# Optimization experiments

Hardware: AMD Instinct MI355X
Metric: run time of the kernel (lower is better)

Reference implementation:

```python
import jax, jax.numpy as jnp
import numpy as np

K = 20
NEG = 0.2      # leaky relu slope
EPS = 1e-5     # layernorm eps


def knn(x, k=K):
    # x: [B, C, N] -> neighbor indices [B, N, k] by largest negative sq-distance
    xt = jnp.swapaxes(x, 1, 2)                      # [B, N, C]
    inner = -2.0 * jnp.einsum('bnc,bcm->bnm', xt, x)
    xx = jnp.sum(x * x, axis=1)                     # [B, N]
    pd = -xx[:, :, None] - inner - xx[:, None, :]   # [B, N, N]
    _, idx = jax.lax.top_k(pd, k)
    return idx


def graph_feature(x, k=K):
    # x: [B, C, N] -> edge features [B, 2C, N, k] = cat(neighbor - center, center)
    xt = jnp.swapaxes(x, 1, 2)                      # [B, N, C]
    idx = knn(x, k)                                 # [B, N, k]
    nbr = jax.vmap(lambda f, i: f[i])(xt, idx)      # [B, N, k, C]
    ctr = jnp.broadcast_to(xt[:, :, None, :], nbr.shape)
    feat = jnp.concatenate([nbr - ctr, ctr], axis=-1)
    return jnp.transpose(feat, (0, 3, 1, 2))


def lrelu(x):
    return jnp.where(x >= 0, x, NEG * x)


def conv1x1(x, w):
    # x: [B, C, N, k], w: [O, C]  (BatchNorm2d in eval with default stats == identity)
    return jnp.einsum('oc,bcnk->bonk', w, x)


def layernorm(x, g, b):
    m = jnp.mean(x, axis=-1, keepdims=True)
    v = jnp.var(x, axis=-1, keepdims=True)
    return (x - m) * jax.lax.rsqrt(v + EPS) * g + b


def l2n(x):
    return x / jnp.linalg.norm(x, axis=1, keepdims=True)


def fc_layer(x, w, bias, g, beta):
    # l2-normalize -> Linear -> LayerNorm -> LeakyReLU (fc_layer with norm=True, bn=True)
    x = l2n(x)
    x = x @ w.T
    if bias is not None:
        x = x + bias
    return lrelu(layernorm(x, g, beta))


def transform_net(f0, tw1, tw2, tw3, tfc1_w, tfc1_g, tfc1_b, tfc2_w, tfc2_bias, tfc2_g, tfc2_b, tfc3_w, tfc3_b):
    # f0: [B, 6, N, k]
    h = lrelu(conv1x1(f0, tw1))                     # [B, 64, N, k]
    h = lrelu(conv1x1(h, tw2))                      # [B, 128, N, k]
    h = jnp.max(h, axis=-1, keepdims=True)          # [B, 128, N, 1]
    h = lrelu(conv1x1(h, tw3))                      # [B, 1024, N, 1]
    h = jnp.max(h, axis=2)[:, :, 0]                 # [B, 1024]
    h = fc_layer(h, tfc1_w, None, tfc1_g, tfc1_b)   # dgcnn: fc1 bias=False
    h = fc_layer(h, tfc2_w, tfc2_bias, tfc2_g, tfc2_b)
    h = h @ tfc3_w.T + tfc3_b                       # [B, 9]
    h = h + jnp.eye(3, dtype=h.dtype).reshape(9)
    return h.reshape(-1, 3, 3)


def setup_inputs() -> dict:
    key = jax.random.key(0)
    ks = jax.random.split(key, 16)

    def w(k, o, i):
        return jax.random.normal(k, (o, i), dtype=jnp.float32) / np.sqrt(i)

    inp = {
        'x': jax.random.normal(ks[0], (16, 3, 1024), dtype=jnp.float32),
        # transform_net params
        'tw1': w(ks[1], 64, 6),
        'tw2': w(ks[2], 128, 64),
        'tw3': w(ks[3], 1024, 128),
        'tfc1_w': w(ks[4], 512, 1024),
        'tfc1_g': jnp.ones((512,), jnp.float32),
        'tfc1_b': jnp.zeros((512,), jnp.float32),
        'tfc2_w': w(ks[5], 256, 512),
        'tfc2_bias': jnp.zeros((256,), jnp.float32),
        'tfc2_g': jnp.ones((256,), jnp.float32),
        'tfc2_b': jnp.zeros((256,), jnp.float32),
        'tfc3_w': w(ks[6], 9, 256) * 0.01,
        'tfc3_b': jnp.zeros((9,), jnp.float32),
        # EdgeConv params (1x1 convs, bias=False for dgcnn)
        'w1': w(ks[7], 64, 6),
        'w2': w(ks[8], 64, 128),
        'w3': w(ks[9], 128, 128),
        'w4': w(ks[10], 256, 256),
        'w5': w(ks[11], 1024, 512),
    }
    return inp


def reference(x, tw1, tw2, tw3, tfc1_w, tfc1_g, tfc1_b, tfc2_w, tfc2_bias, tfc2_g, tfc2_b,
              tfc3_w, tfc3_b, w1, w2, w3, w4, w5):
    # spatial transform from first graph feature
    f0 = graph_feature(x)                           # [B, 6, N, k]
    t = transform_net(f0, tw1, tw2, tw3, tfc1_w, tfc1_g, tfc1_b,
                      tfc2_w, tfc2_bias, tfc2_g, tfc2_b, tfc3_w, tfc3_b)
    x = jnp.einsum('bij,bjn->bin', t, x)            # [B, 3, N]

    # 4 EdgeConv blocks: graph_feature -> 1x1 conv (+BN identity) -> lrelu -> max over k
    x1 = jnp.max(lrelu(conv1x1(graph_feature(x), w1)), axis=-1)    # [B, 64, N]
    x2 = jnp.max(lrelu(conv1x1(graph_feature(x1), w2)), axis=-1)   # [B, 64, N]
    x3 = jnp.max(lrelu(conv1x1(graph_feature(x2), w3)), axis=-1)   # [B, 128, N]
    x4 = jnp.max(lrelu(conv1x1(graph_feature(x3), w4)), axis=-1)   # [B, 256, N]

    xc = jnp.concatenate([x1, x2, x3, x4], axis=1)  # [B, 512, N]
    x5 = lrelu(jnp.einsum('oc,bcn->bon', w5, xc))   # [B, 1024, N]
    return jnp.max(x5, axis=-1)                     # [B, 1024] global feature
```

## Files before the change

kernel.cpp:

```cpp
#include <hip/hip_runtime.h>
#include <math.h>

#define BATCH 16
#define NPTS 1024
#define KNN 20

__device__ __forceinline__ float lrelu(float v) { return v >= 0.f ? v : 0.2f * v; }

typedef __attribute__((ext_vector_type(8))) short bf16x8;
typedef __attribute__((ext_vector_type(4))) float f32x4;

__device__ __forceinline__ ushort f2bf(float f) {
  union { float f; unsigned u; } v; v.f = f;
  unsigned r = (v.u + 0x7FFFu + ((v.u >> 16) & 1u)) >> 16;
  return (ushort)r;
}

__device__ __forceinline__ unsigned wave_min_u32(unsigned v) {
  unsigned t;
  t = (unsigned)__builtin_amdgcn_update_dpp((int)v, (int)v, 0x111, 0xf, 0xf, false);
  v = t < v ? t : v;
  t = (unsigned)__builtin_amdgcn_update_dpp((int)v, (int)v, 0x112, 0xf, 0xf, false);
  v = t < v ? t : v;
  t = (unsigned)__builtin_amdgcn_update_dpp((int)v, (int)v, 0x114, 0xf, 0xf, false);
  v = t < v ? t : v;
  t = (unsigned)__builtin_amdgcn_update_dpp((int)v, (int)v, 0x118, 0xf, 0xf, false);
  v = t < v ? t : v;
  t = (unsigned)__builtin_amdgcn_update_dpp((int)v, (int)v, 0x142, 0xf, 0xf, false);
  v = t < v ? t : v;
  t = (unsigned)__builtin_amdgcn_update_dpp((int)v, (int)v, 0x143, 0xf, 0xf, false);
  v = t < v ? t : v;
  return (unsigned)__builtin_amdgcn_readlane((int)v, 63);
}

__global__ __launch_bounds__(256)
void prep_all_kernel(const float* __restrict__ tw1, const float* __restrict__ w1,
                     const float* __restrict__ w2, const float* __restrict__ w3,
                     const float* __restrict__ w4, const float* __restrict__ w5,
                     const float* __restrict__ tw2, const float* __restrict__ tw3,
                     float* __restrict__ tw1aT, float* __restrict__ tw1dT,
                     float* __restrict__ w1aT, float* __restrict__ w1dT,
                     float* __restrict__ w2aT, float* __restrict__ w2dT,
                     float* __restrict__ w3aT, float* __restrict__ w3dT,
                     ushort* __restrict__ w4a_bf, ushort* __restrict__ w4d_bf,
                     ushort* __restrict__ w5_bf,
                     float* __restrict__ tw2T, float* __restrict__ tw3T) {
  int g = blockIdx.x * 256 + threadIdx.x;
  if (g < 524288) { w5_bf[g] = f2bf(w5[g]); return; }
  g -= 524288;
  if (g < 131072) { int c = g >> 10, o = g & 1023; tw3T[g] = tw3[o * 128 + c]; return; }
  g -= 131072;
  if (g < 32768) {
    int o = g >> 7, c = g & 127;
    float a = w4[o * 256 + c], bb = w4[o * 256 + 128 + c];
    w4a_bf[g] = f2bf(a); w4d_bf[g] = f2bf(bb - a);
    return;
  }
  g -= 32768;
  if (g < 8192) {
    int c = g >> 7, o = g & 127;
    float a = w3[o * 128 + c], bb = w3[o * 128 + 64 + c];
    w3aT[g] = a; w3dT[g] = bb - a;
    return;
  }
  g -= 8192;
  if (g < 8192) { int c = g >> 7, o = g & 127; tw2T[g] = tw2[o * 64 + c]; return; }
  g -= 8192;
  if (g < 4096) {
    int c = g >> 6, o = g & 63;
    float a = w2[o * 128 + c], bb = w2[o * 128 + 64 + c];
    w2aT[g] = a; w2dT[g] = bb - a;
    return;
  }
  g -= 4096;
  if (g < 192) {
    int c = g >> 6, o = g & 63;
    float a = tw1[o * 6 + c], bb = tw1[o * 6 + 3 + c];
    tw1aT[g] = a; tw1dT[g] = bb - a;
    return;
  }
  g -= 192;
  if (g < 192) {
    int c = g >> 6, o = g & 63;
    float a = w1[o * 6 + c], bb = w1[o * 6 + 3 + c];
    w1aT[g] = a; w1dT[g] = bb - a;
  }
}

template<int C, int NO>
__global__ __launch_bounds__(256)
void knn_dual_kernel(const float* __restrict__ X, long sxb,
                     const float* __restrict__ xx, int* __restrict__ idxout,
                     const float* __restrict__ WaT, const float* __restrict__ WdT,
                     int ldW, float* __restrict__ outY, float* __restrict__ outZ,
                     long sob, int son) {
  __shared__ __align__(16) char smem[16384];
  const int gid = blockIdx.x;
  const int tid = threadIdx.x;

  if (gid < 1024) {
    float (*sc4)[NPTS] = reinterpret_cast<float (*)[NPTS]>(smem);
    const int b = gid >> 6, i0 = (gid & 63) * 16;
    const float* Xb = X + (size_t)b * sxb;
    const int j0 = tid * 4;
    float acc[16][4];
    #pragma unroll
    for (int q = 0; q < 16; ++q)
      #pragma unroll
      for (int u = 0; u < 4; ++u) acc[q][u] = 0.f;
    float4 xxjv = make_float4(0.f, 0.f, 0.f, 0.f);
    for (int c = 0; c < C; ++c) {
      const float4 xv = *reinterpret_cast<const float4*>(Xb + (size_t)c * NPTS + j0);
      if (C == 3) {
        xxjv.x = fmaf(xv.x, xv.x, xxjv.x);
        xxjv.y = fmaf(xv.y, xv.y, xxjv.y);
        xxjv.z = fmaf(xv.z, xv.z, xxjv.z);
        xxjv.w = fmaf(xv.w, xv.w, xxjv.w);
      }
      const float* xr = Xb + (size_t)c * NPTS + i0;
      #pragma unroll
      for (int q = 0; q < 16; ++q) {
        const float xiq = xr[q];
        acc[q][0] = fmaf(xiq, xv.x, acc[q][0]);
        acc[q][1] = fmaf(xiq, xv.y, acc[q][1]);
        acc[q][2] = fmaf(xiq, xv.z, acc[q][2]);
        acc[q][3] = fmaf(xiq, xv.w, acc[q][3]);
      }
    }
    float4 xxj;
    if (C == 3) xxj = xxjv;
    else xxj = *reinterpret_cast<const float4*>(xx + b * NPTS + j0);
    const int wv = tid >> 6, lane = tid & 63;
    unsigned ku[4][16];

    #pragma unroll
    for (int r = 0; r < 4; ++r) {
      if (r > 0) __syncthreads();
      #pragma unroll
      for (int q = 0; q < 4; ++q) {
        const int qq = r * 4 + q;
        float4 st;
        st.x = fmaf(-2.f, acc[qq][0], xxj.x);
        st.y = fmaf(-2.f, acc[qq][1], xxj.y);
        st.z = fmaf(-2.f, acc[qq][2], xxj.z);
        st.w = fmaf(-2.f, acc[qq][3], xxj.w);
        *reinterpret_cast<float4*>(&sc4[q][j0]) = st;
      }
      __syncthreads();
      #pragma unroll
      for (int s = 0; s < 16; ++s) {
        const unsigned u = __float_as_uint(sc4[wv][lane + 64 * s]);
        ku[r][s] = u ^ ((unsigned)((int)u >> 31) | 0x80000000u);
      }
    }

    unsigned c1s[4], c2s[4]; int c1j[4], c2j[4];
    #pragma unroll
    for (int r = 0; r < 4; ++r) {
      unsigned b1 = 0xFFFFFFFFu, b2 = 0xFFFFFFFFu; int s1 = 0, s2 = 0;
      #pragma unroll
      for (int s = 0; s < 16; ++s) {
        const unsigned k = ku[r][s];
        const bool a1 = k < b1, a2 = k < b2;
        const unsigned n1 = a1 ? k : b1;  const int ns1 = a1 ? s : s1;
        const unsigned n2 = a1 ? b1 : (a2 ? k : b2);
        const int ns2 = a1 ? s1 : (a2 ? s : s2);
        b1 = n1; s1 = ns1; b2 = n2; s2 = ns2;
      }
      c1s[r] = b1; c1j[r] = lane + (s1 << 6);
      c2s[r] = b2; c2j[r] = lane + (s2 << 6);
    }
    const unsigned INVS = 0xFFFFFFFFu;
    int my[4] = {0, 0, 0, 0};
    for (int t = 0; t < KNN; ++t) {
      unsigned ws[4]; int wl[4], jw[4];
      #pragma unroll
      for (int r = 0; r < 4; ++r) ws[r] = wave_min_u32(c1s[r]);
      #pragma unroll
      for (int r = 0; r < 4; ++r) wl[r] = __ffsll((long long)__ballot(c1s[r] == ws[r])) - 1;
      #pragma unroll
      for (int r = 0; r < 4; ++r) jw[r] = __builtin_amdgcn_readlane(c1j[r], wl[r]);
      if (lane == t) {
        #pragma unroll
        for (int r = 0; r < 4; ++r) my[r] = jw[r];
      }
      bool cons = false;
      #pragma unroll
      for (int r = 0; r < 4; ++r) {
        const bool win = (lane == wl[r]);
        c1s[r] = win ? c2s[r] : c1s[r];
        c1j[r] = win ? c2j[r] : c1j[r];
        c2s[r] = win ? INVS : c2s[r];
        cons = cons || (c1s[r] == INVS);
      }
      if (__any(cons)) {
        #pragma unroll
        for (int r = 0; r < 4; ++r) {
          if (c1s[r] == INVS) {
            unsigned m1 = INVS, m2 = INVS; int r1 = 0, r2 = 0;
            #pragma unroll
            for (int s = 0; s < 16; ++s) {
              const unsigned k = ku[r][s];
              const bool ok = k > ws[r];
              const bool a1 = ok && (k < m1), a2 = ok && (k < m2);
              const unsigned nm1 = a1 ? k : m1;  const int nr1 = a1 ? s : r1;
              const unsigned nm2 = a1 ? m1 : (a2 ? k : m2);
              const int nr2 = a1 ? r1 : (a2 ? s : r2);
              m1 = nm1; r1 = nr1; m2 = nm2; r2 = nr2;
            }
            c1s[r] = (m1 == INVS) ? 0xFFFFFFFEu : m1;  c1j[r] = lane + (r1 << 6);
            c2s[r] = (m2 == INVS) ? 0xFFFFFFFEu : m2;  c2j[r] = lane + (r2 << 6);
          }
        }
      }
    }
    if (lane < KNN) {
      #pragma unroll
      for (int r = 0; r < 4; ++r)
        idxout[(size_t)(b * NPTS + i0 + r * 4 + wv) * KNN + lane] = my[r];
    }
  } else {
    float (*Xs)[64]  = reinterpret_cast<float (*)[64]>(smem);
    float (*Was)[64] = reinterpret_cast<float (*)[64]>(smem + 4096);
    float (*Wds)[64] = reinterpret_cast<float (*)[64]>(smem + 8192);
    const int g2 = gid - 1024;
    const int bx = g2 & 15;
    const int rest = g2 >> 4;
    const int oy = rest % NO;
    const int b = rest / NO;
    const int n0 = bx * 64, o0 = oy * 64;
    const int lr = tid & 63;
    const int c4 = (tid >> 6) * 4;
    const int tn = tid & 15, to = tid >> 4;
    float accY[4][4], accZ[4][4];
    #pragma unroll
    for (int i = 0; i < 4; ++i)
      #pragma unroll
      for (int j = 0; j < 4; ++j) { accY[i][j] = 0.f; accZ[i][j] = 0.f; }

    const size_t xbase = (size_t)b * sxb;
    for (int k0 = 0; k0 < C; k0 += 16) {
      #pragma unroll
      for (int u = 0; u < 4; ++u) {
        int c = k0 + c4 + u;
        float xv = 0.f, wa = 0.f, wd = 0.f;
        if (c < C) {
          xv = X[xbase + (size_t)(n0 + lr) + (size_t)c * NPTS];
          wa = WaT[(size_t)c * ldW + o0 + lr];
          wd = WdT[(size_t)c * ldW + o0 + lr];
        }
        Xs[c4 + u][lr] = xv;
        Was[c4 + u][lr] = wa;
        Wds[c4 + u][lr] = wd;
      }
      __syncthreads();
      #pragma unroll
      for (int kk = 0; kk < 16; ++kk) {
        const float4 xa = *reinterpret_cast<const float4*>(&Xs[kk][tn * 4]);
        const float4 wav = *reinterpret_cast<const float4*>(&Was[kk][to * 4]);
        const float4 wdv = *reinterpret_cast<const float4*>(&Wds[kk][to * 4]);
        const float xr[4] = {xa.x, xa.y, xa.z, xa.w};
        const float war[4] = {wav.x, wav.y, wav.z, wav.w};
        const float wdr[4] = {wdv.x, wdv.y, wdv.z, wdv.w};
        #pragma unroll
        for (int i = 0; i < 4; ++i)
          #pragma unroll
          for (int j = 0; j < 4; ++j) {
            accY[i][j] = fmaf(xr[i], war[j], accY[i][j]);
            accZ[i][j] = fmaf(xr[i], wdr[j], accZ[i][j]);
          }
      }
      __syncthreads();
    }
    #pragma unroll
    for (int i = 0; i < 4; ++i) {
      const size_t base = (size_t)b * sob + (size_t)(n0 + tn * 4 + i) * son + o0 + to * 4;
      *reinterpret_cast<float4*>(&outY[base]) =
        make_float4(accY[i][0], accY[i][1], accY[i][2], accY[i][3]);
      *reinterpret_cast<float4*>(&outZ[base]) =
        make_float4(accZ[i][0], accZ[i][1], accZ[i][2], accZ[i][3]);
    }
  }
}

__global__ __launch_bounds__(256)
void knn_mfma_kernel(const float* __restrict__ Xt, long sxb,
                     const float* __restrict__ xx, int* __restrict__ idxout,
                     const ushort* __restrict__ Xg,
                     const ushort* __restrict__ w4a, const ushort* __restrict__ w4d,
                     float* __restrict__ ybuf, float* __restrict__ zbuf) {
  __shared__ __align__(16) char smem[32768];
  const int gid = blockIdx.x;
  const int tid = threadIdx.x;

  if (gid < 1024) {
    float (*sc4)[NPTS] = reinterpret_cast<float (*)[NPTS]>(smem);
    const int b = gid >> 6, i0 = (gid & 63) * 16;
    const float* Xb = Xt + (size_t)b * sxb;
    const int j0 = tid * 4;
    float acc[16][4];
    #pragma unroll
    for (int q = 0; q < 16; ++q)
      #pragma unroll
      for (int u = 0; u < 4; ++u) acc[q][u] = 0.f;
    for (int c = 0; c < 128; ++c) {
      const float4 xv = *reinterpret_cast<const float4*>(Xb + (size_t)c * NPTS + j0);
      const float* xr = Xb + (size_t)c * NPTS + i0;
      #pragma unroll
      for (int q = 0; q < 16; ++q) {
        const float xiq = xr[q];
        acc[q][0] = fmaf(xiq, xv.x, acc[q][0]);
        acc[q][1] = fmaf(xiq, xv.y, acc[q][1]);
        acc[q][2] = fmaf(xiq, xv.z, acc[q][2]);
        acc[q][3] = fmaf(xiq, xv.w, acc[q][3]);
      }
    }
    const float4 xxj = *reinterpret_cast<const float4*>(xx + b * NPTS + j0);
    const int wv = tid >> 6, lane = tid & 63;
    unsigned ku[4][16];
    #pragma unroll
    for (int r = 0; r < 4; ++r) {
      if (r > 0) __syncthreads();
      #pragma unroll
      for (int q = 0; q < 4; ++q) {
        const int qq = r * 4 + q;
        float4 st;
        st.x = fmaf(-2.f, acc[qq][0], xxj.x);
        st.y = fmaf(-2.f, acc[qq][1], xxj.y);
        st.z = fmaf(-2.f, acc[qq][2], xxj.z);
        st.w = fmaf(-2.f, acc[qq][3], xxj.w);
        *reinterpret_cast<float4*>(&sc4[q][j0]) = st;
      }
      __syncthreads();
      #pragma unroll
      for (int s = 0; s < 16; ++s) {
        const unsigned u = __float_as_uint(sc4[wv][lane + 64 * s]);
        ku[r][s] = u ^ ((unsigned)((int)u >> 31) | 0x80000000u);
      }
    }
    unsigned c1s[4], c2s[4]; int c1j[4], c2j[4];
    #pragma unroll
    for (int r = 0; r < 4; ++r) {
      unsigned b1 = 0xFFFFFFFFu, b2 = 0xFFFFFFFFu; int s1 = 0, s2 = 0;
      #pragma unroll
      for (int s = 0; s < 16; ++s) {
        const unsigned k = ku[r][s];
        const bool a1 = k < b1, a2 = k < b2;
        const unsigned n1 = a1 ? k : b1;  const int ns1 = a1 ? s : s1;
        const unsigned n2 = a1 ? b1 : (a2 ? k : b2);
        const int ns2 = a1 ? s1 : (a2 ? s : s2);
        b1 = n1; s1 = ns1; b2 = n2; s2 = ns2;
      }
      c1s[r] = b1; c1j[r] = lane + (s1 << 6);
      c2s[r] = b2; c2j[r] = lane + (s2 << 6);
    }
    const unsigned INVS = 0xFFFFFFFFu;
    int my[4] = {0, 0, 0, 0};
    for (int t = 0; t < KNN; ++t) {
      unsigned ws[4]; int wl[4], jw[4];
      #pragma unroll
      for (int r = 0; r < 4; ++r) ws[r] = wave_min_u32(c1s[r]);
      #pragma unroll
      for (int r = 0; r < 4; ++r) wl[r] = __ffsll((long long)__ballot(c1s[r] == ws[r])) - 1;
      #pragma unroll
      for (int r = 0; r < 4; ++r) jw[r] = __builtin_amdgcn_readlane(c1j[r], wl[r]);
      if (lane == t) {
        #pragma unroll
        for (int r = 0; r < 4; ++r) my[r] = jw[r];
      }
      bool cons = false;
      #pragma unroll
      for (int r = 0; r < 4; ++r) {
        const bool win = (lane == wl[r]);
        c1s[r] = win ? c2s[r] : c1s[r];
        c1j[r] = win ? c2j[r] : c1j[r];
        c2s[r] = win ? INVS : c2s[r];
        cons = cons || (c1s[r] == INVS);
      }
      if (__any(cons)) {
        #pragma unroll
        for (int r = 0; r < 4; ++r) {
          if (c1s[r] == INVS) {
            unsigned m1 = INVS, m2 = INVS; int r1 = 0, r2 = 0;
            #pragma unroll
            for (int s = 0; s < 16; ++s) {
              const unsigned k = ku[r][s];
              const bool ok = k > ws[r];
              const bool a1 = ok && (k < m1), a2 = ok && (k < m2);
              const unsigned nm1 = a1 ? k : m1;  const int nr1 = a1 ? s : r1;
              const unsigned nm2 = a1 ? m1 : (a2 ? k : m2);
              const int nr2 = a1 ? r1 : (a2 ? s : r2);
              m1 = nm1; r1 = nr1; m2 = nm2; r2 = nr2;
            }
            c1s[r] = (m1 == INVS) ? 0xFFFFFFFEu : m1;  c1j[r] = lane + (r1 << 6);
            c2s[r] = (m2 == INVS) ? 0xFFFFFFFEu : m2;  c2j[r] = lane + (r2 << 6);
          }
        }
      }
    }
    if (lane < KNN) {
      #pragma unroll
      for (int r = 0; r < 4; ++r)
        idxout[(size_t)(b * NPTS + i0 + r * 4 + wv) * KNN + lane] = my[r];
    }
  } else {
    char* As = smem;
    char* Bs = smem + 16384;
    int g2 = gid - 1024;
    const ushort* Wg = (g2 < 256) ? w4a : w4d;
    float* outp = (g2 < 256) ? ybuf : zbuf;
    g2 &= 255;
    const int bx = g2 & 7, oy = (g2 >> 3) & 1, b = g2 >> 4;
    const int n0 = bx * 128, o0 = oy * 128;
    const int lane = tid & 63;
    const int wrow = (tid >> 6) >> 1, wcol = (tid >> 6) & 1;
    f32x4 acc[4][4];
    #pragma unroll
    for (int i = 0; i < 4; ++i)
      #pragma unroll
      for (int j = 0; j < 4; ++j)
        #pragma unroll
        for (int r = 0; r < 4; ++r) acc[i][j][r] = 0.f;

    const ushort* Xb = Xg + (size_t)b * NPTS * 512;
    for (int kb = 0; kb < 128; kb += 64) {
      #pragma unroll
      for (int i = 0; i < 4; ++i) {
        const int idx = i * 256 + tid;
        const int n = idx >> 3, kc = idx & 7;
        const bf16x8 xv = *reinterpret_cast<const bf16x8*>(&Xb[(size_t)(n0 + n) * 512 + kb + kc * 8]);
        const bf16x8 wvv = *reinterpret_cast<const bf16x8*>(&Wg[(size_t)(o0 + n) * 128 + kb + kc * 8]);
        const int ad = n * 128 + ((kc * 16) ^ ((n & 7) << 4));
        *reinterpret_cast<bf16x8*>(As + ad) = xv;
        *reinterpret_cast<bf16x8*>(Bs + ad) = wvv;
      }
      __syncthreads();
      #pragma unroll
      for (int s = 0; s < 2; ++s) {
        bf16x8 af[4], bfr[4];
        const int klane = (s * 64 + ((lane >> 4) << 4));
        #pragma unroll
        for (int f = 0; f < 4; ++f) {
          const int nl = wrow * 64 + f * 16 + (lane & 15);
          af[f] = *reinterpret_cast<const bf16x8*>(As + nl * 128 + (klane ^ ((nl & 7) << 4)));
          const int ol = wcol * 64 + f * 16 + (lane & 15);
          bfr[f] = *reinterpret_cast<const bf16x8*>(Bs + ol * 128 + (klane ^ ((ol & 7) << 4)));
        }
        #pragma unroll
        for (int i = 0; i < 4; ++i)
          #pragma unroll
          for (int j = 0; j < 4; ++j)
            acc[i][j] = __builtin_amdgcn_mfma_f32_16x16x32_bf16(af[i], bfr[j], acc[i][j], 0, 0, 0);
      }
      __syncthreads();
    }
    #pragma unroll
    for (int i = 0; i < 4; ++i)
      #pragma unroll
      for (int r = 0; r < 4; ++r) {
        const int n = n0 + wrow * 64 + i * 16 + ((lane >> 4) << 2) + r;
        #pragma unroll
        for (int j = 0; j < 4; ++j) {
          const int o = o0 + wcol * 64 + j * 16 + (lane & 15);
          outp[(size_t)b * NPTS * 256 + (size_t)n * 256 + o] = acc[i][j][r];
        }
      }
  }
}

template<int EPI>
__global__ __launch_bounds__(256)
void gemm128_kernel(const float* __restrict__ X, long sxb, int scN,
                    const float* __restrict__ WT, int ldW, int C,
                    float* __restrict__ out, int sob, int son, int snb) {
  __shared__ __align__(16) float Xs[16][128];
  __shared__ __align__(16) float Ws[16][128];
  __shared__ __align__(16) float red[16][132];
  const int b = blockIdx.z;
  const int n0 = blockIdx.x * 128, o0 = blockIdx.y * 128;
  const int tid = threadIdx.x;
  const int tn = tid & 15, to = tid >> 4;
  float acc[8][8];
  #pragma unroll
  for (int i = 0; i < 8; ++i)
    #pragma unroll
    for (int j = 0; j < 8; ++j) acc[i][j] = 0.f;

  const size_t xbase = (size_t)b * sxb;
  for (int c0 = 0; c0 < C; c0 += 16) {
    #pragma unroll
    for (int it = 0; it < 2; ++it) {
      const int task = tid + it * 256;
      const int kk = task >> 5, n4 = (task & 31) * 4;
      *reinterpret_cast<float4*>(&Xs[kk][n4]) =
        *reinterpret_cast<const float4*>(&X[xbase + (size_t)(c0 + kk) * scN + n0 + n4]);
      *reinterpret_cast<float4*>(&Ws[kk][n4]) =
        *reinterpret_cast<const float4*>(&WT[(size_t)(c0 + kk) * ldW + o0 + n4]);
    }
    __syncthreads();
    #pragma unroll
    for (int kk = 0; kk < 16; ++kk) {
      const float4 xa0 = *reinterpret_cast<const float4*>(&Xs[kk][tn * 4]);
      const float4 xa1 = *reinterpret_cast<const float4*>(&Xs[kk][64 + tn * 4]);
      const float4 wb0 = *reinterpret_cast<const float4*>(&Ws[kk][to * 4]);
      const float4 wb1 = *reinterpret_cast<const float4*>(&Ws[kk][64 + to * 4]);
      const float xr[8] = {xa0.x, xa0.y, xa0.z, xa0.w, xa1.x, xa1.y, xa1.z, xa1.w};
      const float wr[8] = {wb0.x, wb0.y, wb0.z, wb0.w, wb1.x, wb1.y, wb1.z, wb1.w};
      #pragma unroll
      for (int i = 0; i < 8; ++i)
        #pragma unroll
        for (int j = 0; j < 8; ++j) acc[i][j] = fmaf(xr[i], wr[j], acc[i][j]);
    }
    __syncthreads();
  }

  if (EPI == 0) {
    #pragma unroll
    for (int i = 0; i < 8; ++i) {
      const int n = n0 + (i >> 2) * 64 + tn * 4 + (i & 3);
      float4 s0 = make_float4(acc[i][0], acc[i][1], acc[i][2], acc[i][3]);
      float4 s1 = make_float4(acc[i][4], acc[i][5], acc[i][6], acc[i][7]);
      *reinterpret_cast<float4*>(&out[(size_t)b * sob + (size_t)n * son + o0 + to * 4]) = s0;
      *reinterpret_cast<float4*>(&out[(size_t)b * sob + (size_t)n * son + o0 + 64 + to * 4]) = s1;
    }
  } else {
    #pragma unroll
    for (int j = 0; j < 8; ++j) {
      float m = lrelu(acc[0][j]);
      #pragma unroll
      for (int i = 1; i < 8; ++i) m = fmaxf(m, lrelu(acc[i][j]));
      red[tn][(j >> 2) * 64 + to * 4 + (j & 3)] = m;
    }
    __syncthreads();
    if (tid < 128) {
      float m = red[0][tid];
      #pragma unroll
      for (int t = 1; t < 16; ++t) m = fmaxf(m, red[t][tid]);
      out[(size_t)b * sob + (size_t)blockIdx.x * snb + o0 + tid] = m;
    }
  }
}

template<int EPI>
__global__ __launch_bounds__(256)
void gemm_mfma_kernel(const ushort* __restrict__ Xg, long sxb, int ldX,
                      const ushort* __restrict__ Wg, int ldW, int K,
                      float* __restrict__ out, long sob, int son, int snb) {
  __shared__ __align__(16) ushort As[128 * 64];
  __shared__ __align__(16) ushort Bs[128 * 64];
  __shared__ float red[2][128];
  const int b = blockIdx.z;
  const int n0 = blockIdx.x * 128, o0 = blockIdx.y * 128;
  const int tid = threadIdx.x;
  const int lane = tid & 63;
  const int wrow = (tid >> 6) >> 1, wcol = (tid >> 6) & 1;
  f32x4 acc[4][4];
  #pragma unroll
  for (int i = 0; i < 4; ++i)
    #pragma unroll
    for (int j = 0; j < 4; ++j)
      #pragma unroll
      for (int r = 0; r < 4; ++r) acc[i][j][r] = 0.f;

  const ushort* Xb = Xg + (size_t)b * sxb;
  for (int kb = 0; kb < K; kb += 64) {
    #pragma unroll
    for (int i = 0; i < 4; ++i) {
      const int idx = i * 256 + tid;
      const int n = idx >> 3, kc = idx & 7;
      const bf16x8 xv = *reinterpret_cast<const bf16x8*>(&Xb[(size_t)(n0 + n) * ldX + kb + kc * 8]);
      const bf16x8 wv = *reinterpret_cast<const bf16x8*>(&Wg[(size_t)(o0 + n) * ldW + kb + kc * 8]);
      const int ad = n * 128 + ((kc * 16) ^ ((n & 7) << 4));
      *reinterpret_cast<bf16x8*>((char*)As + ad) = xv;
      *reinterpret_cast<bf16x8*>((char*)Bs + ad) = wv;
    }
    __syncthreads();
    #pragma unroll
    for (int s = 0; s < 2; ++s) {
      bf16x8 af[4], bfr[4];
      const int klane = (s * 64 + ((lane >> 4) << 4));
      #pragma unroll
      for (int f = 0; f < 4; ++f) {
        const int nl = wrow * 64 + f * 16 + (lane & 15);
        af[f] = *reinterpret_cast<const bf16x8*>((char*)As + nl * 128 + (klane ^ ((nl & 7) << 4)));
        const int ol = wcol * 64 + f * 16 + (lane & 15);
        bfr[f] = *reinterpret_cast<const bf16x8*>((char*)Bs + ol * 128 + (klane ^ ((ol & 7) << 4)));
      }
      #pragma unroll
      for (int i = 0; i < 4; ++i)
        #pragma unroll
        for (int j = 0; j < 4; ++j)
          acc[i][j] = __builtin_amdgcn_mfma_f32_16x16x32_bf16(af[i], bfr[j], acc[i][j], 0, 0, 0);
    }
    __syncthreads();
  }

  if (EPI == 0) {
    #pragma unroll
    for (int i = 0; i < 4; ++i)
      #pragma unroll
      for (int r = 0; r < 4; ++r) {
        const int n = n0 + wrow * 64 + i * 16 + ((lane >> 4) << 2) + r;
        #pragma unroll
        for (int j = 0; j < 4; ++j) {
          const int o = o0 + wcol * 64 + j * 16 + (lane & 15);
          out[(size_t)b * sob + (size_t)n * son + o] = acc[i][j][r];
        }
      }
  } else {
    #pragma unroll
    for (int j = 0; j < 4; ++j) {
      float m = -3.4e38f;
      #pragma unroll
      for (int i = 0; i < 4; ++i)
        #pragma unroll
        for (int r = 0; r < 4; ++r) m = fmaxf(m, lrelu(acc[i][j][r]));
      m = fmaxf(m, __shfl_xor(m, 16));
      m = fmaxf(m, __shfl_xor(m, 32));
      if (lane < 16) red[wrow][wcol * 64 + j * 16 + lane] = m;
    }
    __syncthreads();
    if (tid < 128) {
      float m = fmaxf(red[0][tid], red[1][tid]);
      out[(size_t)b * sob + (size_t)blockIdx.x * snb + o0 + tid] = m;
    }
  }
}

template<int O, int TI>
__global__ __launch_bounds__(256)
void edge_max_cn_kernel(const float* __restrict__ y, const float* __restrict__ z,
                        const int* __restrict__ idx, float* __restrict__ outCN,
                        float* __restrict__ xx, ushort* __restrict__ xbf, int choff) {
  __shared__ float tile[TI][O + 1];
  const int b = blockIdx.y;
  const int i0 = blockIdx.x * TI;
  const int wv = threadIdx.x >> 6, lane = threadIdx.x & 63;
  constexpr int OSEG = O / 64;
  constexpr int ROUNDS = TI * OSEG / 4;
  for (int r = 0; r < ROUNDS; ++r) {
    const int item = r * 4 + wv;
    const int il = item / OSEG, os = item - il * OSEG;
    const int i = i0 + il, o = os * 64 + lane;
    const int* ip = idx + (size_t)(b * NPTS + i) * KNN;
    const float zv = z[(size_t)(b * NPTS + i) * O + o];
    float m = -3.4e38f;
    #pragma unroll
    for (int t = 0; t < KNN; ++t) {
      int j = ip[t];
      float v = y[(size_t)(b * NPTS + j) * O + o] + zv;
      m = fmaxf(m, lrelu(v));
    }
    tile[il][o] = m;
    xbf[(size_t)(b * NPTS + i) * 512 + choff + o] = f2bf(m);
  }
  __syncthreads();
  if (xx != nullptr && threadIdx.x < TI) {
    const int il = threadIdx.x;
    float s = 0.f;
    #pragma unroll
    for (int o = 0; o < O; ++o) { float v = tile[il][o]; s = fmaf(v, v, s); }
    xx[b * NPTS + i0 + il] = s;
  }
  for (int e = threadIdx.x; e < TI * O; e += 256) {
    const int o = e / TI, il = e - o * TI;
    outCN[(size_t)b * 512 * NPTS + (size_t)o * NPTS + i0 + il] = tile[il][o];
  }
}

__global__ __launch_bounds__(256)
void h12_gemm_kernel(const float* __restrict__ ya, const float* __restrict__ zb,
                     const int* __restrict__ idx, const float* __restrict__ tw2T,
                     float* __restrict__ h2m) {
  __shared__ __align__(16) float h1s[80][68];
  __shared__ __align__(16) float ws[64][128];
  __shared__ __align__(16) float zbs[4][64];
  __shared__ float ot[128][4];
  __shared__ int idxs[4][KNN];
  const int b = blockIdx.y;
  const int i0 = blockIdx.x * 4;
  const int tid = threadIdx.x;

  #pragma unroll
  for (int it = 0; it < 8; ++it) {
    const int f = tid + it * 256;
    *reinterpret_cast<float4*>(&ws[0][0] + f * 4) =
      *reinterpret_cast<const float4*>(tw2T + (size_t)f * 4);
  }
  if (tid < 64) {
    const int p = tid >> 4, cq = (tid & 15) * 4;
    *reinterpret_cast<float4*>(&zbs[p][cq]) =
      *reinterpret_cast<const float4*>(&zb[(size_t)(b * NPTS + i0 + p) * 64 + cq]);
  }
  if (tid >= 64 && tid < 64 + 4 * KNN) {
    const int e = tid - 64;
    idxs[e / KNN][e % KNN] = idx[(size_t)(b * NPTS + i0) * KNN + e];
  }
  __syncthreads();

  #pragma unroll
  for (int it = 0; it < 5; ++it) {
    const int task = tid + it * 256;
    const int e = task >> 4, cq = (task & 15) * 4;
    const int p = e / KNN, t = e - p * KNN;
    const int j = idxs[p][t];
    const float4 yv = *reinterpret_cast<const float4*>(&ya[(size_t)(b * NPTS + j) * 64 + cq]);
    const float4 zv = *reinterpret_cast<const float4*>(&zbs[p][cq]);
// ... 265 lines not shown
```

Before: 690.1 us.

## Restructure KNN top-k to 16-lane row groups with per-lane top-3 candidates

Replaces the wave-wide (64-lane) top-k selection, where each wave handled 4 query rows serially, with a scheme that assigns each query row to a 16-lane DPP row: each lane holds 64 candidates and keeps a top-3 list, and row_min16 performs the reduction with 4 DPP steps instead of 6 plus a readlane. The distance computation is also retiled into 4 column chunks of 256, with a padded (264-wide) shared scratch, so fewer accumulators are live at once. The aim is to cut the serial cost of the 20 selection rounds and reduce register pressure. In exchange each lane keeps 64 keys in registers, and refills now scan 64 values.

```diff
diff --git a/kernel.cpp b/kernel.cpp
--- a/kernel.cpp
+++ b/kernel.cpp
@@ -16,21 +16,126 @@
   return (ushort)r;
 }
 
-__device__ __forceinline__ unsigned wave_min_u32(unsigned v) {
+__device__ __forceinline__ unsigned row_min16(unsigned v) {
   unsigned t;
-  t = (unsigned)__builtin_amdgcn_update_dpp((int)v, (int)v, 0x111, 0xf, 0xf, false);
+  t = (unsigned)__builtin_amdgcn_update_dpp((int)v, (int)v, 0x121, 0xf, 0xf, false);
   v = t < v ? t : v;
-  t = (unsigned)__builtin_amdgcn_update_dpp((int)v, (int)v, 0x112, 0xf, 0xf, false);
+  t = (unsigned)__builtin_amdgcn_update_dpp((int)v, (int)v, 0x122, 0xf, 0xf, false);
   v = t < v ? t : v;
-  t = (unsigned)__builtin_amdgcn_update_dpp((int)v, (int)v, 0x114, 0xf, 0xf, false);
+  t = (unsigned)__builtin_amdgcn_update_dpp((int)v, (int)v, 0x124, 0xf, 0xf, false);
   v = t < v ? t : v;
-  t = (unsigned)__builtin_amdgcn_update_dpp((int)v, (int)v, 0x118, 0xf, 0xf, false);
+  t = (unsigned)__builtin_amdgcn_update_dpp((int)v, (int)v, 0x128, 0xf, 0xf, false);
   v = t < v ? t : v;
-  t = (unsigned)__builtin_amdgcn_update_dpp((int)v, (int)v, 0x142, 0xf, 0xf, false);
-  v = t < v ? t : v;
-  t = (unsigned)__builtin_amdgcn_update_dpp((int)v, (int)v, 0x143, 0xf, 0xf, false);
-  v = t < v ? t : v;
-  return (unsigned)__builtin_amdgcn_readlane((int)v, 63);
+  return v;
+}
+
+template<int C>
+__device__ __forceinline__ void knn16_body(const float* __restrict__ Xb,
+                                           const float* __restrict__ xxb,
+                                           int* __restrict__ idxq,
+                                           float (*sc)[264],
+                                           int i0, int tid) {
+  const int w = tid >> 6;
+  const int jp = tid & 63;
+  const int g = tid >> 4;
+  const int li = tid & 15;
+  const int lw = tid & 63;
+  unsigned ku[64];
+
+  #pragma unroll
+  for (int jc = 0; jc < 4; ++jc) {
+    if (jc > 0) __syncthreads();
+    const int j0 = jc * 256 + jp * 4;
+    float acc[4][4];
+    #pragma unroll
+    for (int q = 0; q < 4; ++q)
+      #pragma unroll
+      for (int u = 0; u < 4; ++u) acc[q][u] = 0.f;
+    float4 xxv = make_float4(0.f, 0.f, 0.f, 0.f);
+    for (int c = 0; c < C; ++c) {
+      const float4 xj = *reinterpret_cast<const float4*>(Xb + (size_t)c * NPTS + j0);
+      if (C == 3) {
+        xxv.x = fmaf(xj.x, xj.x, xxv.x);
+        xxv.y = fmaf(xj.y, xj.y, xxv.y);
+        xxv.z = fmaf(xj.z, xj.z, xxv.z);
+        xxv.w = fmaf(xj.w, xj.w, xxv.w);
+      }
+      const float* xq = Xb + (size_t)c * NPTS + i0 + w * 4;
+      #pragma unroll
+      for (int q = 0; q < 4; ++q) {
+        const float s = xq[q];
+        acc[q][0] = fmaf(s, xj.x, acc[q][0]);
+        acc[q][1] = fmaf(s, xj.y, acc[q][1]);
+        acc[q][2] = fmaf(s, xj.z, acc[q][2]);
+        acc[q][3] = fmaf(s, xj.w, acc[q][3]);
+      }
+    }
+    float4 xxj;
+    if (C == 3) xxj = xxv;
+    else xxj = *reinterpret_cast<const float4*>(xxb + j0);
+    #pragma unroll
+    for (int q = 0; q < 4; ++q) {
+      float4 st;
+      st.x = fmaf(-2.f, acc[q][0], xxj.x);
+      st.y = fmaf(-2.f, acc[q][1], xxj.y);
+      st.z = fmaf(-2.f, acc[q][2], xxj.z);
+      st.w = fmaf(-2.f, acc[q][3], xxj.w);
+      *reinterpret_cast<float4*>(&sc[w * 4 + q][jp * 4]) = st;
+    }
+    __syncthreads();
+    #pragma unroll
+    for (int sp = 0; sp < 16; ++sp) {
+      const unsigned u = __float_as_uint(sc[g][li + 16 * sp]);
+      ku[jc * 16 + sp] = u ^ ((unsigned)((int)u >> 31) | 0x80000000u);
+    }
+  }
+
+  const unsigned INVS = 0xFFFFFFFFu;
+  unsigned b1 = INVS, b2 = INVS, b3 = INVS; int s1 = 0, s2 = 0, s3 = 0;
+  #pragma unroll
+  for (int s = 0; s < 64; ++s) {
+    const unsigned k = ku[s];
+    const bool a1 = k < b1, a2 = k < b2, a3 = k < b3;
+    const unsigned n1 = a1 ? k : b1;             const int t1 = a1 ? s : s1;
+    const unsigned n2 = a1 ? b1 : (a2 ? k : b2); const int t2 = a1 ? s1 : (a2 ? s : s2);
+    const unsigned n3 = (a1 || a2) ? b2 : (a3 ? k : b3);
+    const int t3 = (a1 || a2) ? s2 : (a3 ? s : s3);
+    b1 = n1; s1 = t1; b2 = n2; s2 = t2; b3 = n3; s3 = t3;
+  }
+  unsigned c1s = b1, c2s = b2, c3s = b3;
+  int c1j = li + (s1 << 4), c2j = li + (s2 << 4), c3j = li + (s3 << 4);
+
+  const unsigned long long rowmask = 0xFFFFull << (lw & 48);
+  const unsigned long long lowmask = (lw == 0) ? 0ull : ((1ull << lw) - 1ull);
+  for (int t = 0; t < KNN; ++t) {
+    const unsigned rm = row_min16(c1s);
+    const bool pred = (c1s == rm);
+    const unsigned long long bal = __ballot(pred);
+    const bool win = pred && ((bal & rowmask & lowmask) == 0ull);
+    if (win) idxq[g * KNN + t] = c1j;
+    c1s = win ? c2s : c1s;  c1j = win ? c2j : c1j;
+    c2s = win ? c3s : c2s;  c2j = win ? c3j : c2j;
+    c3s = win ? INVS : c3s;
+    if (__any(c1s == INVS)) {
+      if (c1s == INVS) {
+        unsigned m1 = INVS, m2 = INVS, m3 = INVS; int r1 = 0, r2 = 0, r3 = 0;
+        #pragma unroll
+        for (int s = 0; s < 64; ++s) {
+          const unsigned k = ku[s];
+          const bool ok = k > rm;
+          const bool a1 = ok && (k < m1), a2 = ok && (k < m2), a3 = ok && (k < m3);
+          const unsigned n1 = a1 ? k : m1;             const int t1 = a1 ? s : r1;
+          const unsigned n2 = a1 ? m1 : (a2 ? k : m2); const int t2 = a1 ? r1 : (a2 ? s : r2);
+          const unsigned n3 = (a1 || a2) ? m2 : (a3 ? k : m3);
+          const int t3 = (a1 || a2) ? r2 : (a3 ? s : r3);
+          m1 = n1; r1 = t1; m2 = n2; r2 = t2; m3 = n3; r3 = t3;
+        }
+        c1s = (m1 == INVS) ? 0xFFFFFFFEu : m1;  c1j = li + (r1 << 4);
+        c2s = (m2 == INVS) ? 0xFFFFFFFEu : m2;  c2j = li + (r2 << 4);
+        c3s = (m3 == INVS) ? 0xFFFFFFFEu : m3;  c3j = li + (r3 << 4);
+      }
+    }
+  }
 }
 
 __global__ __launch_bounds__(256)
@@ -94,131 +199,15 @@
                      const float* __restrict__ WaT, const float* __restrict__ WdT,
                      int ldW, float* __restrict__ outY, float* __restrict__ outZ,
                      long sob, int son) {
-  __shared__ __align__(16) char smem[16384];
+  __shared__ __align__(16) char smem[16896];
   const int gid = blockIdx.x;
   const int tid = threadIdx.x;
 
   if (gid < 1024) {
-    float (*sc4)[NPTS] = reinterpret_cast<float (*)[NPTS]>(smem);
+    float (*sc)[264] = reinterpret_cast<float (*)[264]>(smem);
     const int b = gid >> 6, i0 = (gid & 63) * 16;
-    const float* Xb = X + (size_t)b * sxb;
-    const int j0 = tid * 4;
-    float acc[16][4];
-    #pragma unroll
-    for (int q = 0; q < 16; ++q)
-      #pragma unroll
-      for (int u = 0; u < 4; ++u) acc[q][u] = 0.f;
-    float4 xxjv = make_float4(0.f, 0.f, 0.f, 0.f);
-    for (int c = 0; c < C; ++c) {
-      const float4 xv = *reinterpret_cast<const float4*>(Xb + (size_t)c * NPTS + j0);
-      if (C == 3) {
-        xxjv.x = fmaf(xv.x, xv.x, xxjv.x);
-        xxjv.y = fmaf(xv.y, xv.y, xxjv.y);
-        xxjv.z = fmaf(xv.z, xv.z, xxjv.z);
-        xxjv.w = fmaf(xv.w, xv.w, xxjv.w);
-      }
-      const float* xr = Xb + (size_t)c * NPTS + i0;
-      #pragma unroll
-      for (int q = 0; q < 16; ++q) {
-        const float xiq = xr[q];
-        acc[q][0] = fmaf(xiq, xv.x, acc[q][0]);
-        acc[q][1] = fmaf(xiq, xv.y, acc[q][1]);
-        acc[q][2] = fmaf(xiq, xv.z, acc[q][2]);
-        acc[q][3] = fmaf(xiq, xv.w, acc[q][3]);
-      }
-    }
-    float4 xxj;
-    if (C == 3) xxj = xxjv;
-    else xxj = *reinterpret_cast<const float4*>(xx + b * NPTS + j0);
-    const int wv = tid >> 6, lane = tid & 63;
-    unsigned ku[4][16];
-
-    #pragma unroll
-    for (int r = 0; r < 4; ++r) {
-      if (r > 0) __syncthreads();
-      #pragma unroll
-      for (int q = 0; q < 4; ++q) {
-        const int qq = r * 4 + q;
-        float4 st;
-        st.x = fmaf(-2.f, acc[qq][0], xxj.x);
-        st.y = fmaf(-2.f, acc[qq][1], xxj.y);
-        st.z = fmaf(-2.f, acc[qq][2], xxj.z);
-        st.w = fmaf(-2.f, acc[qq][3], xxj.w);
-        *reinterpret_cast<float4*>(&sc4[q][j0]) = st;
-      }
-      __syncthreads();
-      #pragma unroll
-      for (int s = 0; s < 16; ++s) {
-        const unsigned u = __float_as_uint(sc4[wv][lane + 64 * s]);
-        ku[r][s] = u ^ ((unsigned)((int)u >> 31) | 0x80000000u);
-      }
-    }
-
-    unsigned c1s[4], c2s[4]; int c1j[4], c2j[4];
-    #pragma unroll
-    for (int r = 0; r < 4; ++r) {
-      unsigned b1 = 0xFFFFFFFFu, b2 = 0xFFFFFFFFu; int s1 = 0, s2 = 0;
-      #pragma unroll
-      for (int s = 0; s < 16; ++s) {
-        const unsigned k = ku[r][s];
-        const bool a1 = k < b1, a2 = k < b2;
-        const unsigned n1 = a1 ? k : b1;  const int ns1 = a1 ? s : s1;
-        const unsigned n2 = a1 ? b1 : (a2 ? k : b2);
-        const int ns2 = a1 ? s1 : (a2 ? s : s2);
-        b1 = n1; s1 = ns1; b2 = n2; s2 = ns2;
-      }
-      c1s[r] = b1; c1j[r] = lane + (s1 << 6);
-      c2s[r] = b2; c2j[r] = lane + (s2 << 6);
-    }
-    const unsigned INVS = 0xFFFFFFFFu;
-    int my[4] = {0, 0, 0, 0};
-    for (int t = 0; t < KNN; ++t) {
-      unsigned ws[4]; int wl[4], jw[4];
-      #pragma unroll
-      for (int r = 0; r < 4; ++r) ws[r] = wave_min_u32(c1s[r]);
-      #pragma unroll
-      for (int r = 0; r < 4; ++r) wl[r] = __ffsll((long long)__ballot(c1s[r] == ws[r])) - 1;
-      #pragma unroll
-      for (int r = 0; r < 4; ++r) jw[r] = __builtin_amdgcn_readlane(c1j[r], wl[r]);
-      if (lane == t) {
-        #pragma unroll
-        for (int r = 0; r < 4; ++r) my[r] = jw[r];
-      }
-      bool cons = false;
-      #pragma unroll
-      for (int r = 0; r < 4; ++r) {
-        const bool win = (lane == wl[r]);
-        c1s[r] = win ? c2s[r] : c1s[r];
-        c1j[r] = win ? c2j[r] : c1j[r];
-        c2s[r] = win ? INVS : c2s[r];
-        cons = cons || (c1s[r] == INVS);
-      }
-      if (__any(cons)) {
-        #pragma unroll
-        for (int r = 0; r < 4; ++r) {
-          if (c1s[r] == INVS) {
-            unsigned m1 = INVS, m2 = INVS; int r1 = 0, r2 = 0;
-            #pragma unroll
-            for (int s = 0; s < 16; ++s) {
-              const unsigned k = ku[r][s];
-              const bool ok = k > ws[r];
-              const bool a1 = ok && (k < m1), a2 = ok && (k < m2);
-              const unsigned nm1 = a1 ? k : m1;  const int nr1 = a1 ? s : r1;
-              const unsigned nm2 = a1 ? m1 : (a2 ? k : m2);
-              const int nr2 = a1 ? r1 : (a2 ? s : r2);
-              m1 = nm1; r1 = nr1; m2 = nm2; r2 = nr2;
-            }
-            c1s[r] = (m1 == INVS) ? 0xFFFFFFFEu : m1;  c1j[r] = lane + (r1 << 6);
-            c2s[r] = (m2 == INVS) ? 0xFFFFFFFEu : m2;  c2j[r] = lane + (r2 << 6);
-          }
-        }
-      }
-    }
-    if (lane < KNN) {
-      #pragma unroll
-      for (int r = 0; r < 4; ++r)
-        idxout[(size_t)(b * NPTS + i0 + r * 4 + wv) * KNN + lane] = my[r];
-    }
+    knn16_body<C>(X + (size_t)b * sxb, (C == 3) ? nullptr : (xx + b * NPTS),
+                  idxout + (size_t)(b * NPTS + i0) * KNN, sc, i0, tid);
   } else {
     float (*Xs)[64]  = reinterpret_cast<float (*)[64]>(smem);
     float (*Was)[64] = reinterpret_cast<float (*)[64]>(smem + 4096);
@@ -294,115 +283,10 @@
   const int tid = threadIdx.x;
 
   if (gid < 1024) {
-    float (*sc4)[NPTS] = reinterpret_cast<float (*)[NPTS]>(smem);
+    float (*sc)[264] = reinterpret_cast<float (*)[264]>(smem);
     const int b = gid >> 6, i0 = (gid & 63) * 16;
-    const float* Xb = Xt + (size_t)b * sxb;
-    const int j0 = tid * 4;
-    float acc[16][4];
-    #pragma unroll
-    for (int q = 0; q < 16; ++q)
-      #pragma unroll
-      for (int u = 0; u < 4; ++u) acc[q][u] = 0.f;
-    for (int c = 0; c < 128; ++c) {
-      const float4 xv = *reinterpret_cast<const float4*>(Xb + (size_t)c * NPTS + j0);
-      const float* xr = Xb + (size_t)c * NPTS + i0;
-      #pragma unroll
-      for (int q = 0; q < 16; ++q) {
-        const float xiq = xr[q];
-        acc[q][0] = fmaf(xiq, xv.x, acc[q][0]);
-        acc[q][1] = fmaf(xiq, xv.y, acc[q][1]);
-        acc[q][2] = fmaf(xiq, xv.z, acc[q][2]);
-        acc[q][3] = fmaf(xiq, xv.w, acc[q][3]);
-      }
-    }
-    const float4 xxj = *reinterpret_cast<const float4*>(xx + b * NPTS + j0);
-    const int wv = tid >> 6, lane = tid & 63;
-    unsigned ku[4][16];
-    #pragma unroll
-    for (int r = 0; r < 4; ++r) {
-      if (r > 0) __syncthreads();
-      #pragma unroll
-      for (int q = 0; q < 4; ++q) {
-        const int qq = r * 4 + q;
-        float4 st;
-        st.x = fmaf(-2.f, acc[qq][0], xxj.x);
-        st.y = fmaf(-2.f, acc[qq][1], xxj.y);
-        st.z = fmaf(-2.f, acc[qq][2], xxj.z);
-        st.w = fmaf(-2.f, acc[qq][3], xxj.w);
-        *reinterpret_cast<float4*>(&sc4[q][j0]) = st;
-      }
-      __syncthreads();
-      #pragma unroll
-      for (int s = 0; s < 16; ++s) {
-        const unsigned u = __float_as_uint(sc4[wv][lane + 64 * s]);
-        ku[r][s] = u ^ ((unsigned)((int)u >> 31) | 0x80000000u);
-      }
-    }
-    unsigned c1s[4], c2s[4]; int c1j[4], c2j[4];
-    #pragma unroll
-    for (int r = 0; r < 4; ++r) {
-      unsigned b1 = 0xFFFFFFFFu, b2 = 0xFFFFFFFFu; int s1 = 0, s2 = 0;
-      #pragma unroll
-      for (int s = 0; s < 16; ++s) {
-        const unsigned k = ku[r][s];
-        const bool a1 = k < b1, a2 = k < b2;
-        const unsigned n1 = a1 ? k : b1;  const int ns1 = a1 ? s : s1;
-        const unsigned n2 = a1 ? b1 : (a2 ? k : b2);
-        const int ns2 = a1 ? s1 : (a2 ? s : s2);
-        b1 = n1; s1 = ns1; b2 = n2; s2 = ns2;
-      }
-      c1s[r] = b1; c1j[r] = lane + (s1 << 6);
-      c2s[r] = b2; c2j[r] = lane + (s2 << 6);
-    }
-    const unsigned INVS = 0xFFFFFFFFu;
-    int my[4] = {0, 0, 0, 0};
-    for (int t = 0; t < KNN; ++t) {
-      unsigned ws[4]; int wl[4], jw[4];
-      #pragma unroll
-      for (int r = 0; r < 4; ++r) ws[r] = wave_min_u32(c1s[r]);
-      #pragma unroll
-      for (int r = 0; r < 4; ++r) wl[r] = __ffsll((long long)__ballot(c1s[r] == ws[r])) - 1;
-      #pragma unroll
-      for (int r = 0; r < 4; ++r) jw[r] = __builtin_amdgcn_readlane(c1j[r], wl[r]);
-      if (lane == t) {
-        #pragma unroll
-        for (int r = 0; r < 4; ++r) my[r] = jw[r];
-      }
-      bool cons = false;
-      #pragma unroll
-      for (int r = 0; r < 4; ++r) {
-        const bool win = (lane == wl[r]);
-        c1s[r] = win ? c2s[r] : c1s[r];
-        c1j[r] = win ? c2j[r] : c1j[r];
-        c2s[r] = win ? INVS : c2s[r];
-        cons = cons || (c1s[r] == INVS);
-      }
-      if (__any(cons)) {
-        #pragma unroll
-        for (int r = 0; r < 4; ++r) {
-          if (c1s[r] == INVS) {
-            unsigned m1 = INVS, m2 = INVS; int r1 = 0, r2 = 0;
-            #pragma unroll
-            for (int s = 0; s < 16; ++s) {
-              const unsigned k = ku[r][s];
-              const bool ok = k > ws[r];
-              const bool a1 = ok && (k < m1), a2 = ok && (k < m2);
-              const unsigned nm1 = a1 ? k : m1;  const int nr1 = a1 ? s : r1;
-              const unsigned nm2 = a1 ? m1 : (a2 ? k : m2);
-              const int nr2 = a1 ? r1 : (a2 ? s : r2);
-              m1 = nm1; r1 = nr1; m2 = nm2; r2 = nr2;
-            }
-            c1s[r] = (m1 == INVS) ? 0xFFFFFFFEu : m1;  c1j[r] = lane + (r1 << 6);
-            c2s[r] = (m2 == INVS) ? 0xFFFFFFFEu : m2;  c2j[r] = lane + (r2 << 6);
-          }
-        }
-      }
-    }
-    if (lane < KNN) {
-      #pragma unroll
-      for (int r = 0; r < 4; ++r)
-        idxout[(size_t)(b * NPTS + i0 + r * 4 + wv) * KNN + lane] = my[r];
-    }
+    knn16_body<128>(Xt + (size_t)b * sxb, xx + b * NPTS,
+                    idxout + (size_t)(b * NPTS + i0) * KNN, sc, i0, tid);
   } else {
     char* As = smem;
     char* Bs = smem + 16384;
```

New measurement: 1.049 ms. 1.52x slower.
